# Kernel tuning notes

Measured on AMD Instinct MI355X. Metric: run time of the kernel, lower is better.

## Reference

```python
import jax, jax.numpy as jnp
import numpy as np

B, D_IN = 4096, 1024
E, K = 16, 2
EMB = 256
H1, H2 = 2048, 1024  # hidden_units, hidden_units // 2
O = 512              # num_classes


def setup_inputs() -> dict:
    key = jax.random.key(0)
    ks = jax.random.split(key, 10)
    s = lambda *sh: 1.0 / np.sqrt(sh[-2] if len(sh) > 1 else 1.0)
    return {
        "x":   jax.random.normal(ks[0], (B, D_IN), jnp.float32),
        "Wr":  jax.random.normal(ks[1], (D_IN, EMB), jnp.float32) * (1.0 / np.sqrt(D_IN)),
        "br":  jnp.zeros((EMB,), jnp.float32),
        "emb": jax.random.normal(ks[2], (E, EMB), jnp.float32) * (1.0 / np.sqrt(EMB)),
        "W1":  jax.random.normal(ks[3], (E, D_IN, H1), jnp.float32) * (1.0 / np.sqrt(D_IN)),
        "b1":  jnp.zeros((E, H1), jnp.float32),
        "W2":  jax.random.normal(ks[4], (E, H1, H2), jnp.float32) * (1.0 / np.sqrt(H1)),
        "b2":  jnp.zeros((E, H2), jnp.float32),
        "W3":  jax.random.normal(ks[5], (E, H2, O), jnp.float32) * (1.0 / np.sqrt(H2)),
        "b3":  jnp.zeros((E, O), jnp.float32),
    }


def reference(x, Wr, br, emb, W1, b1, W2, b2, W3, b3):
    # Router query: [B, EMB]
    q = x @ Wr + br
    # Negative squared euclidean distance to expert embeddings -> scores [B, E]
    d2 = jnp.sum(jnp.square(q[:, None, :] - emb[None, :, :]), axis=-1)
    scores = -d2
    gating_probs = jax.nn.softmax(scores, axis=-1)  # [B, E]
    # Top-k selection + renormalized gates
    top_v, top_i = jax.lax.top_k(scores, K)          # [B, K]
    gates = jax.nn.softmax(top_v, axis=-1)           # [B, K]
    # All experts run on full batch (dense), batched over expert axis
    h1 = jax.nn.relu(jnp.einsum('bi,eih->beh', x, W1) + b1)   # [B, E, H1]
    h2 = jax.nn.relu(jnp.einsum('beh,ehm->bem', h1, W2) + b2)  # [B, E, H2]
    out = jnp.einsum('bem,emo->beo', h2, W3) + b3              # [B, E, O]
    # Gather top-k expert outputs per example and combine
    sel = jnp.take_along_axis(out, top_i[:, :, None], axis=1)  # [B, K, O]
    final = jnp.sum(sel * gates[:, :, None], axis=1)           # [B, O]
    return final, q, gating_probs
```

## Files before the change

### kernel.cpp

```cpp
#include <hip/hip_runtime.h>
#include <hip/hip_bf16.h>

using bf16 = __hip_bfloat16;
typedef __attribute__((ext_vector_type(8))) short bf16x8;
typedef __attribute__((ext_vector_type(8))) unsigned short u16x8;
typedef __attribute__((ext_vector_type(4))) float f32x4;

constexpr int BATCH = 4096;
constexpr int D_IN  = 1024;
constexpr int NEXP  = 16;
constexpr int EMB   = 256;
constexpr int H1    = 2048;
constexpr int H2    = 1024;
constexpr int OUTD  = 512;
constexpr int SLOTS = BATCH * 2;
constexpr int SLOTS_PAD = SLOTS + 128;
constexpr int MAX_TILES = SLOTS / 128 + NEXP;
constexpr int BIN_CAP   = MAX_TILES / 8;

constexpr size_t WS_XB     = 0;
constexpr size_t WS_H1     = WS_XB     + (size_t)BATCH * D_IN * 2;
constexpr size_t WS_H2     = WS_H1     + (size_t)SLOTS_PAD * H1 * 2;
constexpr size_t WS_OSL    = WS_H2     + (size_t)SLOTS_PAD * H2 * 2;
constexpr size_t WS_TOPI   = WS_OSL    + (size_t)SLOTS_PAD * OUTD * 4;
constexpr size_t WS_GATES  = WS_TOPI   + (size_t)SLOTS * 4;
constexpr size_t WS_SLOTOF = WS_GATES  + (size_t)SLOTS * 4;
constexpr size_t WS_TOKL   = WS_SLOTOF + (size_t)SLOTS * 4;
constexpr size_t WS_CNT    = WS_TOKL   + (size_t)SLOTS_PAD * 4;
constexpr size_t WS_TMAP   = WS_CNT    + 64 * 4;
constexpr size_t WS_WT     = ((WS_TMAP + (size_t)MAX_TILES * 8) + 255) & ~(size_t)255;

__device__ __forceinline__ unsigned short f2bf(float f) {
    bf16 h = __float2bfloat16(f);
    return __builtin_bit_cast(unsigned short, h);
}

__device__ __forceinline__ void gload16(const unsigned short* g, unsigned short* l) {
    __builtin_amdgcn_global_load_lds(
        (const __attribute__((address_space(1))) unsigned int*)g,
        (__attribute__((address_space(3))) unsigned int*)l, 16, 0, 0);
}

__global__ __launch_bounds__(256) void k_cvt_x(const float* __restrict__ x,
                                               unsigned short* __restrict__ xb) {
    int i = blockIdx.x * 256 + threadIdx.x;
    float4 v = reinterpret_cast<const float4*>(x)[i];
    ushort4 o;
    o.x = f2bf(v.x); o.y = f2bf(v.y); o.z = f2bf(v.z); o.w = f2bf(v.w);
    reinterpret_cast<ushort4*>(xb)[i] = o;
}

__global__ __launch_bounds__(256) void k_wtrans(const float* __restrict__ W,
                                                unsigned short* __restrict__ Wt,
                                                int KD, int ND) {
    __shared__ float Tf[64][65];
    int e = blockIdx.z;
    int n0 = blockIdx.x * 64, k0 = blockIdx.y * 64;
    const float* Wb = W + ((size_t)e * KD + k0) * ND + n0;
    int t  = threadIdx.x;
    int kr = t >> 4, c4 = (t & 15) * 4;
#pragma unroll
    for (int i = 0; i < 4; i++) {
        float4 v = *reinterpret_cast<const float4*>(Wb + (size_t)(kr + i * 16) * ND + c4);
        Tf[kr + i * 16][c4 + 0] = v.x; Tf[kr + i * 16][c4 + 1] = v.y;
        Tf[kr + i * 16][c4 + 2] = v.z; Tf[kr + i * 16][c4 + 3] = v.w;
    }
    __syncthreads();
    unsigned short* Wtb = Wt + ((size_t)e * ND + n0) * KD + k0;
#pragma unroll
    for (int i = 0; i < 2; i++) {
        int idx = t + i * 256;
        int n = idx >> 3, ck = (idx & 7) * 8;
        u16x8 o;
#pragma unroll
        for (int j = 0; j < 8; j++) o[j] = f2bf(Tf[ck + j][n]);
        *reinterpret_cast<u16x8*>(Wtb + (size_t)n * KD + ck) = o;
    }
}

__global__ __launch_bounds__(256) void k_router_gemm(const float* __restrict__ x,
                                                     const float* __restrict__ Wr,
                                                     const float* __restrict__ br,
                                                     float* __restrict__ qout) {
    __shared__ float As[64][17];
    __shared__ float Bs[16][68];
    int mb = blockIdx.x * 64, nb = blockIdx.y * 64;
    int t  = threadIdx.x;
    int tx = t & 15, ty = t >> 4;
    float acc[4][4] = {};
    int arow = t >> 2, ak = (t & 3) * 4;
    int bkr = t >> 4, bnc = (t & 15) * 4;
    for (int kt = 0; kt < D_IN; kt += 16) {
        float4 av = *reinterpret_cast<const float4*>(&x[(size_t)(mb + arow) * D_IN + kt + ak]);
        float4 bv = *reinterpret_cast<const float4*>(&Wr[(size_t)(kt + bkr) * EMB + nb + bnc]);
        As[arow][ak + 0] = av.x; As[arow][ak + 1] = av.y;
        As[arow][ak + 2] = av.z; As[arow][ak + 3] = av.w;
        Bs[bkr][bnc + 0] = bv.x; Bs[bkr][bnc + 1] = bv.y;
        Bs[bkr][bnc + 2] = bv.z; Bs[bkr][bnc + 3] = bv.w;
        __syncthreads();
#pragma unroll
        for (int k = 0; k < 16; k++) {
            float a[4], bb[4];
#pragma unroll
            for (int i = 0; i < 4; i++) a[i] = As[ty * 4 + i][k];
#pragma unroll
            for (int j = 0; j < 4; j++) bb[j] = Bs[k][tx * 4 + j];
#pragma unroll
            for (int i = 0; i < 4; i++)
#pragma unroll
                for (int j = 0; j < 4; j++) acc[i][j] = fmaf(a[i], bb[j], acc[i][j]);
        }
        __syncthreads();
    }
#pragma unroll
    for (int i = 0; i < 4; i++) {
        int row = mb + ty * 4 + i;
        float4 o;
        o.x = acc[i][0] + br[nb + tx * 4 + 0];
        o.y = acc[i][1] + br[nb + tx * 4 + 1];
        o.z = acc[i][2] + br[nb + tx * 4 + 2];
        o.w = acc[i][3] + br[nb + tx * 4 + 3];
        *reinterpret_cast<float4*>(&qout[(size_t)row * EMB + nb + tx * 4]) = o;
    }
}

__global__ __launch_bounds__(256) void k_router_topk(const float* __restrict__ q,
                                                     const float* __restrict__ emb,
                                                     float* __restrict__ gp,
                                                     int* __restrict__ topi,
                                                     float* __restrict__ gates) {
    int b    = blockIdx.x * 4 + (threadIdx.x >> 6);
    int lane = threadIdx.x & 63;
    int e    = lane & 15;
    int seg  = (lane >> 4) * 64;
    const float* qr = q + (size_t)b * EMB + seg;
    const float* er = emb + (size_t)e * EMB + seg;
    float d2 = 0.f;
#pragma unroll 8
    for (int i = 0; i < 64; i++) { float d = qr[i] - er[i]; d2 = fmaf(d, d, d2); }
    d2 += __shfl_xor(d2, 16);
    d2 += __shfl_xor(d2, 32);
    float s = -d2;
    float m = s;
#pragma unroll
    for (int o = 1; o < 16; o <<= 1) m = fmaxf(m, __shfl_xor(m, o));
    float ex  = __expf(s - m);
    float sum = ex;
#pragma unroll
    for (int o = 1; o < 16; o <<= 1) sum += __shfl_xor(sum, o);
    if (lane < 16) gp[(size_t)b * NEXP + lane] = ex / sum;
    float v1 = s; int i1 = e;
#pragma unroll
    for (int o = 1; o < 16; o <<= 1) {
        float ov = __shfl_xor(v1, o); int oi = __shfl_xor(i1, o);
        if (ov > v1 || (ov == v1 && oi < i1)) { v1 = ov; i1 = oi; }
    }
    float s2 = (e == i1) ? -1e30f : s;
    float v2 = s2; int i2 = e;
#pragma unroll
    for (int o = 1; o < 16; o <<= 1) {
        float ov = __shfl_xor(v2, o); int oi = __shfl_xor(i2, o);
        if (ov > v2 || (ov == v2 && oi < i2)) { v2 = ov; i2 = oi; }
    }
    if (lane == 0) {
        topi[b * 2] = i1; topi[b * 2 + 1] = i2;
        float tv  = __expf(v2 - v1);
        float inv = 1.f / (1.f + tv);
        gates[b * 2] = inv; gates[b * 2 + 1] = tv * inv;
    }
}

__global__ void k_zero(int* counts) { if (threadIdx.x < NEXP) counts[threadIdx.x] = 0; }

__global__ __launch_bounds__(256) void k_count(const int* __restrict__ topi, int* __restrict__ counts) {
    int i = blockIdx.x * 256 + threadIdx.x;
    atomicAdd(&counts[topi[i]], 1);
}

__global__ void k_scan(const int* __restrict__ counts, int* __restrict__ offsets,
                       int* __restrict__ cursors, int2* __restrict__ tilemap) {
    if (threadIdx.x != 0) return;
    int off = 0;
    int nt_e[NEXP];
    for (int e = 0; e < NEXP; e++) {
        offsets[e] = off; cursors[e] = off;
        nt_e[e] = (counts[e] + 127) >> 7;
        off += counts[e];
    }
    for (int i = 0; i < MAX_TILES; i++) tilemap[i] = make_int2(-1, 0);
    int binload[8] = {0, 0, 0, 0, 0, 0, 0, 0};
    for (int e = 0; e < NEXP; e++) {
        int rem = nt_e[e], ti = 0;
        while (rem > 0) {
            int b = 0;
            for (int q = 1; q < 8; q++)
                if (binload[q] < binload[b]) b = q;
            int space = BIN_CAP - binload[b];
            if (space <= 0) break;
            int take = (rem < space) ? rem : space;
            for (int i = 0; i < take; i++)
                tilemap[b * BIN_CAP + binload[b] + i] = make_int2(e, ti + i);
            binload[b] += take; ti += take; rem -= take;
        }
    }
}

__global__ __launch_bounds__(256) void k_scatter(const int* __restrict__ topi, int* __restrict__ cursors,
                                                 int* __restrict__ toklist, int* __restrict__ slotof) {
    int i = blockIdx.x * 256 + threadIdx.x;
    int e = topi[i];
    int s = atomicAdd(&cursors[e], 1);
    toklist[s] = i >> 1;
    slotof[i]  = s;
}

template <int KD, int ND, int MODE>
__global__ __launch_bounds__(256, 2) void k_expert_gemm(
    const unsigned short* __restrict__ Xin, const unsigned short* __restrict__ Wt,
    const float* __restrict__ bg, unsigned short* __restrict__ Hout,
    float* __restrict__ Oout, const int* __restrict__ counts,
    const int* __restrict__ offsets, const int* __restrict__ toklist,
    const int2* __restrict__ tilemap) {
    int id   = blockIdx.y * gridDim.x + blockIdx.x;
    int cxcd = id & 7;
    int jj   = id >> 3;
    int y    = cxcd * BIN_CAP + jj % BIN_CAP;
    int xnb  = jj / BIN_CAP;

    int2 tm = tilemap[y];
    int e = tm.x;
    if (e < 0) return;
    int mt  = tm.y;
    int n_e = counts[e];
    if (mt * 128 >= n_e) return;
    int off = offsets[e];
    int n0  = xnb * 128;

    __shared__ __align__(16) unsigned short As[2][128 * 64];
    __shared__ __align__(16) unsigned short Bs[2][128 * 64];

    int t    = threadIdx.x;
    int lane = t & 63;
    int w    = t >> 6;
    int wr   = (w >> 1) * 64;
    int wc   = (w & 1) * 64;

    int srow = lane >> 3;
    int swz  = (lane & 7) ^ srow;
    const unsigned short* asrc[4];
    const unsigned short* bsrc[4];
#pragma unroll
    for (int i = 0; i < 4; i++) {
        int r = i * 32 + w * 8 + srow;
        int g = mt * 128 + r;
        size_t arow;
        if (MODE == 0) {
            int gg = (g < n_e) ? g : (n_e - 1);
            arow = (size_t)toklist[off + gg];
        } else {
            arow = (size_t)(off + g);
        }
        asrc[i] = Xin + arow * KD + swz * 8;
        bsrc[i] = Wt + ((size_t)e * ND + n0 + r) * KD + swz * 8;
    }

    auto STAGE = [&](int buf, int kt) {
#pragma unroll
        for (int i = 0; i < 4; i++) {
            gload16(asrc[i] + kt, &As[buf][(i * 32 + w * 8) * 64] + lane * 8);
            gload16(bsrc[i] + kt, &Bs[buf][(i * 32 + w * 8) * 64] + lane * 8);
        }
    };

    f32x4 acc[4][4];
#pragma unroll
    for (int mi = 0; mi < 4; mi++)
#pragma unroll
        for (int ni = 0; ni < 4; ni++) acc[mi][ni] = {0.f, 0.f, 0.f, 0.f};

    int lr  = lane & 15;
    int lkc = lane >> 4;

    constexpr int T = KD / 64;
    STAGE(0, 0);
    __syncthreads();

    for (int tt = 0; tt < T; tt++) {
        int cur = tt & 1;
        if (tt + 1 < T) STAGE(cur ^ 1, (tt + 1) * 64);
        const char* Ab = (const char*)As[cur];
        const char* Bb = (const char*)Bs[cur];
#pragma unroll
        for (int ks = 0; ks < 2; ks++) {
            bf16x8 a[4], b[4];
#pragma unroll
            for (int mi = 0; mi < 4; mi++) {
                int row = wr + mi * 16 + lr;
                int c   = (lkc + ks * 4) ^ (row & 7);
                a[mi] = *reinterpret_cast<const bf16x8*>(Ab + row * 128 + c * 16);
            }
#pragma unroll
            for (int ni = 0; ni < 4; ni++) {
                int row = wc + ni * 16 + lr;
                int c   = (lkc + ks * 4) ^ (row & 7);
                b[ni] = *reinterpret_cast<const bf16x8*>(Bb + row * 128 + c * 16);
            }
#pragma unroll
            for (int mi = 0; mi < 4; mi++)
#pragma unroll
                for (int ni = 0; ni < 4; ni++)
                    acc[mi][ni] = __builtin_amdgcn_mfma_f32_16x16x32_bf16(a[mi], b[ni], acc[mi][ni], 0, 0, 0);
        }
        if (tt + 1 < T) __syncthreads();
    }

    int rowbase = (lane >> 4) * 4;
#pragma unroll
    for (int ni = 0; ni < 4; ni++) {
        int col = n0 + wc + ni * 16 + lr;
        float bv = bg[(size_t)e * ND + col];
#pragma unroll
        for (int mi = 0; mi < 4; mi++) {
#pragma unroll
            for (int qi = 0; qi < 4; qi++) {
                int g = mt * 128 + wr + mi * 16 + rowbase + qi;
                if (g < n_e) {
                    float v = acc[mi][ni][qi] + bv;
                    if (MODE == 2) {
                        Oout[(size_t)(off + g) * ND + col] = v;
                    } else {
                        v = fmaxf(v, 0.f);
                        Hout[(size_t)(off + g) * ND + col] = f2bf(v);
                    }
                }
            }
        }
    }
}

__global__ __launch_bounds__(128) void k_combine(const float* __restrict__ osl,
                                                 const float* __restrict__ gates,
                                                 const int* __restrict__ slotof,
                                                 float* __restrict__ outf) {
    int b = blockIdx.x;
    int j = threadIdx.x;
    int s0 = slotof[b * 2], s1 = slotof[b * 2 + 1];
    float g0 = gates[b * 2], g1 = gates[b * 2 + 1];
    float4 o0 = reinterpret_cast<const float4*>(osl + (size_t)s0 * OUTD)[j];
    float4 o1 = reinterpret_cast<const float4*>(osl + (size_t)s1 * OUTD)[j];
    float4 r;
    r.x = g0 * o0.x + g1 * o1.x;
    r.y = g0 * o0.y + g1 * o1.y;
    r.z = g0 * o0.z + g1 * o1.z;
    r.w = g0 * o0.w + g1 * o1.w;
    reinterpret_cast<float4*>(outf + (size_t)b * OUTD)[j] = r;
}

extern "C" void kernel_launch(void* const* d_in, const int* in_sizes, int n_in,
                              void* d_out, int out_size, void* d_ws, size_t ws_size,
                              hipStream_t stream) {
    const float* x   = (const float*)d_in[0];
    const float* Wr  = (const float*)d_in[1];
    const float* br  = (const float*)d_in[2];
    const float* emb = (const float*)d_in[3];
    const float* W1  = (const float*)d_in[4];
    const float* b1  = (const float*)d_in[5];
    const float* W2  = (const float*)d_in[6];
    const float* b2  = (const float*)d_in[7];
    const float* W3  = (const float*)d_in[8];
    const float* b3  = (const float*)d_in[9];

    float* out_final = (float*)d_out;
    float* out_q     = out_final + (size_t)BATCH * OUTD;
    float* out_gp    = out_q + (size_t)BATCH * EMB;

    char* ws = (char*)d_ws;
    unsigned short* xb  = (unsigned short*)(ws + WS_XB);
    unsigned short* h1  = (unsigned short*)(ws + WS_H1);
    unsigned short* h2  = (unsigned short*)(ws + WS_H2);
    float* osl    = (float*)(ws + WS_OSL);
    int*   topi   = (int*)(ws + WS_TOPI);
    float* gates  = (float*)(ws + WS_GATES);
    int*   slotof = (int*)(ws + WS_SLOTOF);
    int*   toklist= (int*)(ws + WS_TOKL);
    int*   counts = (int*)(ws + WS_CNT);
    int*   offsets= counts + 16;
    int*   cursors= counts + 32;
    int2*  tilemap= (int2*)(ws + WS_TMAP);
    unsigned short* wt = (unsigned short*)(ws + WS_WT);

    k_cvt_x<<<BATCH * D_IN / 4 / 256, 256, 0, stream>>>(x, xb);
    k_router_gemm<<<dim3(BATCH / 64, EMB / 64), 256, 0, stream>>>(x, Wr, br, out_q);
    k_router_topk<<<BATCH / 4, 256, 0, stream>>>(out_q, emb, out_gp, topi, gates);
    k_zero<<<1, 64, 0, stream>>>(counts);
    k_count<<<SLOTS / 256, 256, 0, stream>>>(topi, counts);
    k_scan<<<1, 64, 0, stream>>>(counts, offsets, cursors, tilemap);
    k_scatter<<<SLOTS / 256, 256, 0, stream>>>(topi, cursors, toklist, slotof);

    k_wtrans<<<dim3(H1 / 64, D_IN / 64, NEXP), 256, 0, stream>>>(W1, wt, D_IN, H1);
    k_expert_gemm<D_IN, H1, 0><<<dim3(H1 / 128, MAX_TILES), 256, 0, stream>>>(
        xb, wt, b1, h1, nullptr, counts, offsets, toklist, tilemap);

    k_wtrans<<<dim3(H2 / 64, H1 / 64, NEXP), 256, 0, stream>>>(W2, wt, H1, H2);
    k_expert_gemm<H1, H2, 1><<<dim3(H2 / 128, MAX_TILES), 256, 0, stream>>>(
        h1, wt, b2, h2, nullptr, counts, offsets, toklist, tilemap);

    k_wtrans<<<dim3(OUTD / 64, H2 / 64, NEXP), 256, 0, stream>>>(W3, wt, H2, OUTD);
    k_expert_gemm<H2, OUTD, 2><<<dim3(OUTD / 128, MAX_TILES), 256, 0, stream>>>(
        h2, wt, b3, nullptr, osl, counts, offsets, toklist, tilemap);

    k_combine<<<BATCH, 128, 0, stream>>>(osl, gates, slotof, out_final);
}
```

Baseline: 415.6 us.

## Split expert GEMMs into full 256x256 tiles plus 128-row remainder tiles

Each expert's token rows are now split into full 256-row tiles, handled by a new 512-thread kernel with a 256x256 output tile, and 128-row remainder tiles, handled by the old 128x128 kernel. The larger tiles raise arithmetic intensity and reuse of operands staged in LDS. The full tiles need no bounds checks. The XCD-aware bin-packing tile map is dropped for a simple sequential map. Trade-offs: double the kernel launches per layer, 128 KB of LDS per 256-tile block, and possibly poor occupancy and tail balance.

After: 481.0 us. +15.8%, slower.

```diff
diff --git a/kernel.cpp b/kernel.cpp
--- a/kernel.cpp
+++ b/kernel.cpp
@@ -14,9 +14,9 @@
 constexpr int H2    = 1024;
 constexpr int OUTD  = 512;
 constexpr int SLOTS = BATCH * 2;
-constexpr int SLOTS_PAD = SLOTS + 128;
-constexpr int MAX_TILES = SLOTS / 128 + NEXP;
-constexpr int BIN_CAP   = MAX_TILES / 8;
+constexpr int SLOTS_PAD = SLOTS + 256;
+constexpr int MAX_TF = SLOTS / 256;
+constexpr int MAX_TR = NEXP * 2;
 
 constexpr size_t WS_XB     = 0;
 constexpr size_t WS_H1     = WS_XB     + (size_t)BATCH * D_IN * 2;
@@ -27,8 +27,9 @@
 constexpr size_t WS_SLOTOF = WS_GATES  + (size_t)SLOTS * 4;
 constexpr size_t WS_TOKL   = WS_SLOTOF + (size_t)SLOTS * 4;
 constexpr size_t WS_CNT    = WS_TOKL   + (size_t)SLOTS_PAD * 4;
-constexpr size_t WS_TMAP   = WS_CNT    + 64 * 4;
-constexpr size_t WS_WT     = ((WS_TMAP + (size_t)MAX_TILES * 8) + 255) & ~(size_t)255;
+constexpr size_t WS_TMAPF  = WS_CNT    + 64 * 4;
+constexpr size_t WS_TMAPR  = WS_TMAPF  + (size_t)MAX_TF * 8;
+constexpr size_t WS_WT     = ((WS_TMAPR + (size_t)MAX_TR * 8) + 255) & ~(size_t)255;
 
 __device__ __forceinline__ unsigned short f2bf(float f) {
     bf16 h = __float2bfloat16(f);
@@ -178,31 +179,24 @@
 }
 
 __global__ void k_scan(const int* __restrict__ counts, int* __restrict__ offsets,
-                       int* __restrict__ cursors, int2* __restrict__ tilemap) {
+                       int* __restrict__ cursors, int2* __restrict__ tmapF,
+                       int2* __restrict__ tmapR) {
     if (threadIdx.x != 0) return;
     int off = 0;
-    int nt_e[NEXP];
     for (int e = 0; e < NEXP; e++) {
         offsets[e] = off; cursors[e] = off;
-        nt_e[e] = (counts[e] + 127) >> 7;
         off += counts[e];
     }
-    for (int i = 0; i < MAX_TILES; i++) tilemap[i] = make_int2(-1, 0);
-    int binload[8] = {0, 0, 0, 0, 0, 0, 0, 0};
+    int ntF = 0, ntR = 0;
     for (int e = 0; e < NEXP; e++) {
-        int rem = nt_e[e], ti = 0;
-        while (rem > 0) {
-            int b = 0;
-            for (int q = 1; q < 8; q++)
-                if (binload[q] < binload[b]) b = q;
-            int space = BIN_CAP - binload[b];
-            if (space <= 0) break;
-            int take = (rem < space) ? rem : space;
-            for (int i = 0; i < take; i++)
-                tilemap[b * BIN_CAP + binload[b] + i] = make_int2(e, ti + i);
-            binload[b] += take; ti += take; rem -= take;
-        }
-    }
+        int c  = counts[e];
+        int nF = c >> 8;
+        for (int i = 0; i < nF; i++) tmapF[ntF++] = make_int2(e, i * 256);
+        int base = nF * 256, rem = c - base;
+        while (rem > 0) { tmapR[ntR++] = make_int2(e, base); base += 128; rem -= 128; }
+    }
+    for (; ntF < MAX_TF; ntF++) tmapF[ntF] = make_int2(-1, 0);
+    for (; ntR < MAX_TR; ntR++) tmapR[ntR] = make_int2(-1, 0);
 }
 
 __global__ __launch_bounds__(256) void k_scatter(const int* __restrict__ topi, int* __restrict__ cursors,
@@ -215,26 +209,132 @@
 }
 
 template <int KD, int ND, int MODE>
-__global__ __launch_bounds__(256, 2) void k_expert_gemm(
+__global__ __launch_bounds__(512, 2) void k_gemm256(
+    const unsigned short* __restrict__ Xin, const unsigned short* __restrict__ Wt,
+    const float* __restrict__ bg, unsigned short* __restrict__ Hout,
+    float* __restrict__ Oout, const int* __restrict__ offsets,
+    const int* __restrict__ toklist, const int2* __restrict__ tmapF) {
+    int2 tm = tmapF[blockIdx.y];
+    int e = tm.x;
+    if (e < 0) return;
+    int base = tm.y;
+    int off  = offsets[e];
+    int n0   = blockIdx.x * 256;
+
+    __shared__ __align__(16) unsigned short As[2][256 * 64];
+    __shared__ __align__(16) unsigned short Bs[2][256 * 64];
+
+    int t    = threadIdx.x;
+    int lane = t & 63;
+    int w    = t >> 6;
+    int wm   = w >> 2;
+    int wn   = w & 3;
+
+    int srow  = t >> 3;
+    int chunk = t & 7;
+    const unsigned short* asrc[4];
+    const unsigned short* bsrc[4];
+#pragma unroll
+    for (int i = 0; i < 4; i++) {
+        int row = i * 64 + srow;
+        int swz = chunk ^ (row & 7);
+        int g   = base + row;
+        size_t arow = (MODE == 0) ? (size_t)toklist[off + g] : (size_t)(off + g);
+        asrc[i] = Xin + arow * KD + swz * 8;
+        bsrc[i] = Wt + ((size_t)e * ND + n0 + row) * KD + swz * 8;
+    }
+
+    auto STAGE = [&](int buf, int kt) {
+#pragma unroll
+        for (int i = 0; i < 4; i++) {
+            gload16(asrc[i] + kt, &As[buf][(i * 64 + w * 8) * 64] + lane * 8);
+            gload16(bsrc[i] + kt, &Bs[buf][(i * 64 + w * 8) * 64] + lane * 8);
+        }
+    };
+
+    f32x4 acc[8][4];
+#pragma unroll
+    for (int mi = 0; mi < 8; mi++)
+#pragma unroll
+        for (int ni = 0; ni < 4; ni++) acc[mi][ni] = {0.f, 0.f, 0.f, 0.f};
+
+    int lr  = lane & 15;
+    int lkc = lane >> 4;
+
+    constexpr int NT = KD / 64;
+    STAGE(0, 0);
+    __syncthreads();
+
+    for (int tt = 0; tt < NT; tt++) {
+        int cur = tt & 1;
+        if (tt + 1 < NT) STAGE(cur ^ 1, (tt + 1) * 64);
+        const char* Ab = (const char*)As[cur];
+        const char* Bb = (const char*)Bs[cur];
+#pragma unroll
+        for (int ks = 0; ks < 2; ks++) {
+            bf16x8 b[4];
+#pragma unroll
+            for (int ni = 0; ni < 4; ni++) {
+                int row = wn * 64 + ni * 16 + lr;
+                int c   = (lkc + ks * 4) ^ (row & 7);
+                b[ni] = *reinterpret_cast<const bf16x8*>(Bb + row * 128 + c * 16);
+            }
+#pragma unroll
+            for (int mq = 0; mq < 2; mq++) {
+                bf16x8 a[4];
+#pragma unroll
+                for (int mi = 0; mi < 4; mi++) {
+                    int row = wm * 128 + mq * 64 + mi * 16 + lr;
+                    int c   = (lkc + ks * 4) ^ (row & 7);
+                    a[mi] = *reinterpret_cast<const bf16x8*>(Ab + row * 128 + c * 16);
+                }
+#pragma unroll
+                for (int mi = 0; mi < 4; mi++)
+#pragma unroll
+                    for (int ni = 0; ni < 4; ni++)
+                        acc[mq * 4 + mi][ni] =
+                            __builtin_amdgcn_mfma_f32_16x16x32_bf16(a[mi], b[ni], acc[mq * 4 + mi][ni], 0, 0, 0);
+            }
+        }
+        if (tt + 1 < NT) __syncthreads();
+    }
+
+    int rowbase = (lane >> 4) * 4;
+#pragma unroll
+    for (int ni = 0; ni < 4; ni++) {
+        int col = n0 + wn * 64 + ni * 16 + lr;
+        float bv = bg[(size_t)e * ND + col];
+#pragma unroll
+        for (int mi = 0; mi < 8; mi++) {
+#pragma unroll
+            for (int qi = 0; qi < 4; qi++) {
+                int g = base + wm * 128 + mi * 16 + rowbase + qi;
+                float v = acc[mi][ni][qi] + bv;
+                if (MODE == 2) {
+                    Oout[(size_t)(off + g) * ND + col] = v;
+                } else {
+                    v = fmaxf(v, 0.f);
+                    Hout[(size_t)(off + g) * ND + col] = f2bf(v);
+                }
+            }
+        }
+    }
+}
+
+template <int KD, int ND, int MODE>
+__global__ __launch_bounds__(256, 2) void k_gemm128(
     const unsigned short* __restrict__ Xin, const unsigned short* __restrict__ Wt,
     const float* __restrict__ bg, unsigned short* __restrict__ Hout,
     float* __restrict__ Oout, const int* __restrict__ counts,
     const int* __restrict__ offsets, const int* __restrict__ toklist,
-    const int2* __restrict__ tilemap) {
-    int id   = blockIdx.y * gridDim.x + blockIdx.x;
-    int cxcd = id & 7;
-    int jj   = id >> 3;
-    int y    = cxcd * BIN_CAP + jj % BIN_CAP;
-    int xnb  = jj / BIN_CAP;
-
-    int2 tm = tilemap[y];
+    const int2* __restrict__ tmapR) {
+    int2 tm = tmapR[blockIdx.y];
     int e = tm.x;
     if (e < 0) return;
-    int mt  = tm.y;
-    int n_e = counts[e];
-    if (mt * 128 >= n_e) return;
-    int off = offsets[e];
-    int n0  = xnb * 128;
+    int base = tm.y;
+    int n_e  = counts[e];
+    int off  = offsets[e];
+    int n0   = blockIdx.x * 128;
 
     __shared__ __align__(16) unsigned short As[2][128 * 64];
     __shared__ __align__(16) unsigned short Bs[2][128 * 64];
@@ -252,7 +352,7 @@
 #pragma unroll
     for (int i = 0; i < 4; i++) {
         int r = i * 32 + w * 8 + srow;
-        int g = mt * 128 + r;
+        int g = base + r;
         size_t arow;
         if (MODE == 0) {
             int gg = (g < n_e) ? g : (n_e - 1);
@@ -281,13 +381,13 @@
     int lr  = lane & 15;
     int lkc = lane >> 4;
 
-    constexpr int T = KD / 64;
+    constexpr int NT = KD / 64;
     STAGE(0, 0);
     __syncthreads();
 
-    for (int tt = 0; tt < T; tt++) {
+    for (int tt = 0; tt < NT; tt++) {
         int cur = tt & 1;
-        if (tt + 1 < T) STAGE(cur ^ 1, (tt + 1) * 64);
+        if (tt + 1 < NT) STAGE(cur ^ 1, (tt + 1) * 64);
         const char* Ab = (const char*)As[cur];
         const char* Bb = (const char*)Bs[cur];
 #pragma unroll
@@ -311,7 +411,7 @@
                 for (int ni = 0; ni < 4; ni++)
                     acc[mi][ni] = __builtin_amdgcn_mfma_f32_16x16x32_bf16(a[mi], b[ni], acc[mi][ni], 0, 0, 0);
         }
-        if (tt + 1 < T) __syncthreads();
+        if (tt + 1 < NT) __syncthreads();
     }
 
     int rowbase = (lane >> 4) * 4;
@@ -323,7 +423,7 @@
         for (int mi = 0; mi < 4; mi++) {
 #pragma unroll
             for (int qi = 0; qi < 4; qi++) {
-                int g = mt * 128 + wr + mi * 16 + rowbase + qi;
+                int g = base + wr + mi * 16 + rowbase + qi;
                 if (g < n_e) {
                     float v = acc[mi][ni][qi] + bv;
                     if (MODE == 2) {
@@ -386,7 +486,8 @@
     int*   counts = (int*)(ws + WS_CNT);
     int*   offsets= counts + 16;
     int*   cursors= counts + 32;
-    int2*  tilemap= (int2*)(ws + WS_TMAP);
+    int2*  tmapF  = (int2*)(ws + WS_TMAPF);
+    int2*  tmapR  = (int2*)(ws + WS_TMAPR);
     unsigned short* wt = (unsigned short*)(ws + WS_WT);
 
     k_cvt_x<<<BATCH * D_IN / 4 / 256, 256, 0, stream>>>(x, xb);
@@ -394,20 +495,26 @@
     k_router_topk<<<BATCH / 4, 256, 0, stream>>>(out_q, emb, out_gp, topi, gates);
     k_zero<<<1, 64, 0, stream>>>(counts);
     k_count<<<SLOTS / 256, 256, 0, stream>>>(topi, counts);
-    k_scan<<<1, 64, 0, stream>>>(counts, offsets, cursors, tilemap);
+    k_scan<<<1, 64, 0, stream>>>(counts, offsets, cursors, tmapF, tmapR);
     k_scatter<<<SLOTS / 256, 256, 0, stream>>>(topi, cursors, toklist, slotof);
 
     k_wtrans<<<dim3(H1 / 64, D_IN / 64, NEXP), 256, 0, stream>>>(W1, wt, D_IN, H1);
-    k_expert_gemm<D_IN, H1, 0><<<dim3(H1 / 128, MAX_TILES), 256, 0, stream>>>(
-        xb, wt, b1, h1, nullptr, counts, offsets, toklist, tilemap);
+    k_gemm256<D_IN, H1, 0><<<dim3(H1 / 256, MAX_TF), 512, 0, stream>>>(
+        xb, wt, b1, h1, nullptr, offsets, toklist, tmapF);
+    k_gemm128<D_IN, H1, 0><<<dim3(H1 / 128, MAX_TR), 256, 0, stream>>>(
+        xb, wt, b1, h1, nullptr, counts, offsets, toklist, tmapR);
 
     k_wtrans<<<dim3(H2 / 64, H1 / 64, NEXP), 256, 0, stream>>>(W2, wt, H1, H2);
-    k_expert_gemm<H1, H2, 1><<<dim3(H2 / 128, MAX_TILES), 256, 0, stream>>>(
-        h1, wt, b2, h2, nullptr, counts, offsets, toklist, tilemap);
+    k_gemm256<H1, H2, 1><<<dim3(H2 / 256, MAX_TF), 512, 0, stream>>>(
+        h1, wt, b2, h2, nullptr, offsets, toklist, tmapF);
+    k_gemm128<H1, H2, 1><<<dim3(H2 / 128, MAX_TR), 256, 0, stream>>>(
+        h1, wt, b2, h2, nullptr, counts, offsets, toklist, tmapR);
 
     k_wtrans<<<dim3(OUTD / 64, H2 / 64, NEXP), 256, 0, stream>>>(W3, wt, H2, OUTD);
-    k_expert_gemm<H2, OUTD, 2><<<dim3(OUTD / 128, MAX_TILES), 256, 0, stream>>>(
-        h2, wt, b3, nullptr, osl, counts, offsets, toklist, tilemap);
+    k_gemm256<H2, OUTD, 2><<<dim3(OUTD / 256, MAX_TF), 512, 0, stream>>>(
+        h2, wt, b3, nullptr, osl, offsets, toklist, tmapF);
+    k_gemm128<H2, OUTD, 2><<<dim3(OUTD / 128, MAX_TR), 256, 0, stream>>>(
+        h2, wt, b3, nullptr, osl, counts, offsets, toklist, tmapR);
 
     k_combine<<<BATCH, 128, 0, stream>>>(osl, gates, slotof, out_final);
 }
```
